# Kernel optimization log

Hardware: AMD Instinct MI355X
Metric: run time of the kernel (lower is better)

The kernel has to match this reference:

```python
import jax, jax.numpy as jnp
import numpy as np

EPS = 1e-5

def _layernorm(x, g, b):
    mu = jnp.mean(x, axis=-1, keepdims=True)
    var = jnp.mean((x - mu) ** 2, axis=-1, keepdims=True)
    return (x - mu) * jax.lax.rsqrt(var + EPS) * g + b


def setup_inputs() -> dict:
    key = jax.random.key(0)
    ks = jax.random.split(key, 16)
    B, N, D = 16, 10000, 64
    H = 4
    s = 0.02
    return {
        "z_m": jax.random.normal(ks[0], (B, N, D), jnp.float32),
        "z_c": jax.random.normal(ks[1], (B, N, D), jnp.float32),
        "z_t": jax.random.normal(ks[2], (B, N, D), jnp.float32),
        "z_cls": jax.random.normal(ks[3], (D,), jnp.float32) * s,
        # MultiheadAttention packed qkv projection: (3D, D) like torch in_proj_weight
        "in_proj_w": jax.random.normal(ks[4], (3 * D, D), jnp.float32) * s,
        "in_proj_b": jnp.zeros((3 * D,), jnp.float32),
        "out_w": jax.random.normal(ks[5], (D, D), jnp.float32) * s,  # torch (out,in)
        "out_b": jnp.zeros((D,), jnp.float32),
        "ln1_g": jnp.ones((D,), jnp.float32),
        "ln1_b": jnp.zeros((D,), jnp.float32),
        "ln2_g": jnp.ones((D,), jnp.float32),
        "ln2_b": jnp.zeros((D,), jnp.float32),
        "w1": jax.random.normal(ks[6], (2 * D, D), jnp.float32) * s,  # Linear(d, 2d), torch layout (out,in)
        "b1": jnp.zeros((2 * D,), jnp.float32),
        "w2": jax.random.normal(ks[7], (D, 2 * D), jnp.float32) * s,  # Linear(2d, d)
        "b2": jnp.zeros((D,), jnp.float32),
    }


def reference(z_m, z_c, z_t, z_cls, in_proj_w, in_proj_b, out_w, out_b,
              ln1_g, ln1_b, ln2_g, ln2_b, w1, b1, w2, b2):
    B, N, D = z_m.shape
    H = 4
    DH = D // H
    # build (B*N, 4, D) token sequences: [cls, mRNA, CNV, Meth]
    cls_tok = jnp.broadcast_to(z_cls, (B, N, 1, D))
    mods = jnp.stack([z_m, z_c, z_t], axis=2)            # (B,N,3,D)
    X = jnp.concatenate([cls_tok, mods], axis=2).reshape(B * N, 4, D)  # (M,4,D)

    xn = _layernorm(X, ln1_g, ln1_b)
    qkv = jnp.einsum('msd,ed->mse', xn, in_proj_w) + in_proj_b  # (M,4,3D)
    q, k, v = jnp.split(qkv, 3, axis=-1)
    # split heads -> (M,H,4,DH)
    def heads(t):
        return t.reshape(-1, 4, H, DH).transpose(0, 2, 1, 3)
    q, k, v = heads(q), heads(k), heads(v)
    scores = jnp.einsum('mhqd,mhkd->mhqk', q, k) / jnp.sqrt(jnp.float32(DH))
    attn = jax.nn.softmax(scores, axis=-1)               # (M,H,4,4)
    ctx = jnp.einsum('mhqk,mhkd->mhqd', attn, v)
    ctx = ctx.transpose(0, 2, 1, 3).reshape(-1, 4, D)
    attn_out = jnp.einsum('msd,ed->mse', ctx, out_w) + out_b
    # torch need_weights=True averages over heads by default -> (M,4,4)
    attn_weights = jnp.mean(attn, axis=1)

    X = X + attn_out
    yn = _layernorm(X, ln2_g, ln2_b)
    h1 = jax.nn.gelu(jnp.einsum('msd,ed->mse', yn, w1) + b1, approximate=False)
    X = X + jnp.einsum('mse,de->msd', h1, w2) + b2

    h_i = X.reshape(B, N, 4, D)[:, :, 0, :]
    return h_i, attn_weights
```

## Files before the change

### kernel.cpp

```cpp
#include <hip/hip_runtime.h>
#include <math.h>


typedef __attribute__((ext_vector_type(8))) short   short8;
typedef __attribute__((ext_vector_type(4))) float   f32x4;
typedef __attribute__((ext_vector_type(4))) unsigned short us4;
typedef __attribute__((ext_vector_type(8))) unsigned short us8;

#define MFMA16(a,b,c) __builtin_amdgcn_mfma_f32_16x16x32_bf16((a),(b),(c),0,0,0)
#define SWZ(b_, r_) (((unsigned)(b_)) ^ ((((unsigned)(r_)) & 7u) << 4))

__device__ __forceinline__ unsigned short f2bf(float f){
  union { float f; unsigned u; } v; v.f = f;
  unsigned r = v.u + 0x7FFFu + ((v.u >> 16) & 1u);
  return (unsigned short)(r >> 16);
}

__device__ __forceinline__ float fast_gelu(float a){
  float y = a * 0.70710678118654752f;
  float z = fabsf(y);
  float t = __frcp_rn(fmaf(0.3275911f, z, 1.f));
  float poly = t * fmaf(t, fmaf(t, fmaf(t, fmaf(t, 1.061405429f, -1.453152027f),
                                        1.421413741f), -0.284496736f), 0.254829592f);
  float e = __expf(-y * y);
  float erfz = 1.f - poly * e;
  float erfy = (y < 0.f) ? -erfz : erfz;
  return 0.5f * a * (1.f + erfy);
}

template<int C>
__device__ __forceinline__ void stage_w(const float* __restrict__ g,
                                        unsigned short* s, int R, int tid){
  for (int i = tid; i < R*C; i += 256){
    int row = i / C;
    s[SWZ((unsigned)i * 2u, row) >> 1] = f2bf(g[i]);
  }
}

__global__ __launch_bounds__(256)
__attribute__((amdgpu_waves_per_eu(2)))
void mt_kernel(const float* __restrict__ z_m, const float* __restrict__ z_c,
               const float* __restrict__ z_t, const float* __restrict__ z_cls,
               const float* __restrict__ ipw, const float* __restrict__ ipb,
               const float* __restrict__ out_w, const float* __restrict__ out_b,
               const float* __restrict__ ln1_g, const float* __restrict__ ln1_b,
               const float* __restrict__ ln2_g, const float* __restrict__ ln2_b,
               const float* __restrict__ w1, const float* __restrict__ b1,
               const float* __restrict__ w2, const float* __restrict__ b2,
               float* __restrict__ h_out, float* __restrict__ aw_out, int M)
{
  __shared__ unsigned short ipw_s[192*64];
  __shared__ unsigned short ow_s [64*64];
  __shared__ unsigned short w1_s [128*64];
  __shared__ unsigned short w2_s [64*128];
  __shared__ unsigned short xn_s [4*16*64];
  __shared__ unsigned short ctx_s[16*64];
  __shared__ unsigned short yn_s [16*64];
  __shared__ unsigned short h1_s [16*128];

  const int tid = threadIdx.x;
  const int w   = tid >> 6;
  const int l   = tid & 63;
  const int p   = l >> 4;
  const int c16 = l & 15;

  stage_w<64 >(ipw,   ipw_s, 192, tid);
  stage_w<64 >(out_w, ow_s,   64, tid);
  stage_w<64 >(w1,    w1_s,  128, tid);
  stage_w<128>(w2,    w2_s,   64, tid);
  __syncthreads();

  const int d0A = (l & 3) * 16;
  float ln1g[16], ln1b[16];
  #pragma unroll
  for (int i = 0; i < 16; ++i){ ln1g[i] = ln1_g[d0A+i]; ln1b[i] = ln1_b[d0A+i]; }
  float ipb_r[12];
  #pragma unroll
  for (int n = 0; n < 12; ++n) ipb_r[n] = ipb[c16 + 16*n];
  float zcob[16], ln2g[16], ln2b[16];
  #pragma unroll
  for (int mt = 0; mt < 4; ++mt)
    #pragma unroll
    for (int r = 0; r < 4; ++r){
      int e = 16*mt + 4*p + r;
      zcob[mt*4+r] = z_cls[e] + out_b[e];
      ln2g[mt*4+r] = ln2_g[e];  ln2b[mt*4+r] = ln2_b[e];
    }
  float b1r[8];
  #pragma unroll
  for (int tt = 0; tt < 2; ++tt)
    #pragma unroll
    for (int r = 0; r < 4; ++r) b1r[tt*4+r] = b1[16*(2*w+tt) + 4*p + r];
  float b2r[4];
  #pragma unroll
  for (int r = 0; r < 4; ++r) b2r[r] = b2[16*w + 4*p + r];

  unsigned short* xw = xn_s + w*1024;

  const int nT = M >> 4;
  for (int T = blockIdx.x; T < nT; T += gridDim.x){

    {
      const int t  = l >> 2;
      const int sq_ = t & 3;
      const int g  = t >> 2;
      const int m  = T*16 + 4*w + g;
      const float* srcp;
      if      (sq_ == 0) srcp = z_cls + d0A;
      else if (sq_ == 1) srcp = z_m + (size_t)m*64 + d0A;
      else if (sq_ == 2) srcp = z_c + (size_t)m*64 + d0A;
      else               srcp = z_t + (size_t)m*64 + d0A;
      float xv[16];
      #pragma unroll
      for (int i = 0; i < 4; ++i){
        float4 q4 = ((const float4*)srcp)[i];
        xv[4*i+0]=q4.x; xv[4*i+1]=q4.y; xv[4*i+2]=q4.z; xv[4*i+3]=q4.w;
      }
      float sm = 0.f;
      #pragma unroll
      for (int i = 0; i < 16; ++i) sm += xv[i];
      sm += __shfl_xor(sm, 1); sm += __shfl_xor(sm, 2);
      float mu = sm * (1.f/64.f);
      float sq = 0.f;
      #pragma unroll
      for (int i = 0; i < 16; ++i){ float d = xv[i]-mu; sq = fmaf(d,d,sq); }
      sq += __shfl_xor(sq, 1); sq += __shfl_xor(sq, 2);
      float rstd = 1.f / sqrtf(sq * (1.f/64.f) + 1e-5f);
      us8 v0, v1;
      #pragma unroll
      for (int i = 0; i < 8; ++i)
        v0[i] = f2bf(fmaf((xv[i]-mu)*rstd, ln1g[i], ln1b[i]));
      #pragma unroll
      for (int i = 0; i < 8; ++i)
        v1[i] = f2bf(fmaf((xv[8+i]-mu)*rstd, ln1g[8+i], ln1b[8+i]));
      unsigned b0 = (unsigned)(t*64 + d0A) * 2u;
      *(us8*)&xw[SWZ(b0,      t) >> 1] = v0;
      *(us8*)&xw[SWZ(b0 + 16, t) >> 1] = v1;
    }
    __syncthreads();

    f32x4 acc[12];
    #pragma unroll
    for (int n = 0; n < 12; ++n) acc[n] = (f32x4){0.f,0.f,0.f,0.f};
    {
      short8 a0 = *(const short8*)&xw[SWZ((c16*64 +      8*p)*2, c16) >> 1];
      short8 a1 = *(const short8*)&xw[SWZ((c16*64 + 32 + 8*p)*2, c16) >> 1];
      #pragma unroll
      for (int n = 0; n < 12; ++n){
        int e = c16 + 16*n;
        short8 b0 = *(const short8*)&ipw_s[SWZ((e*64 +      8*p)*2, e) >> 1];
        short8 b1v= *(const short8*)&ipw_s[SWZ((e*64 + 32 + 8*p)*2, e) >> 1];
        acc[n] = MFMA16(a0, b0, acc[n]);
        acc[n] = MFMA16(a1, b1v, acc[n]);
      }
      #pragma unroll
      for (int n = 0; n < 12; ++n){
        float bi = ipb_r[n];
        #pragma unroll
        for (int r = 0; r < 4; ++r) acc[n][r] += bi;
      }
    }

    float awm[16];
    #pragma unroll
    for (int i = 0; i < 16; ++i) awm[i] = 0.f;
    float ctx4[4];
    #pragma unroll
    for (int h = 0; h < 4; ++h){
      float sc[16];
      #pragma unroll
      for (int q = 0; q < 4; ++q)
        #pragma unroll
        for (int u = 0; u < 4; ++u) sc[q*4+u] = acc[h][q] * acc[4+h][u];
      #pragma unroll
      for (int st = 0; st < 4; ++st){
        const int mask = 1 << st;
        #pragma unroll
        for (int i = 0; i < 16; ++i) sc[i] += __shfl_xor(sc[i], mask);
      }
      #pragma unroll
      for (int q = 0; q < 4; ++q){
        float s0 = sc[4*q+0]*0.25f, s1 = sc[4*q+1]*0.25f,
              s2 = sc[4*q+2]*0.25f, s3 = sc[4*q+3]*0.25f;
        float mx = fmaxf(fmaxf(s0,s1), fmaxf(s2,s3));
        s0 = __expf(s0-mx); s1 = __expf(s1-mx); s2 = __expf(s2-mx); s3 = __expf(s3-mx);
        float inv = 1.f/(s0+s1+s2+s3);
        s0*=inv; s1*=inv; s2*=inv; s3*=inv;
        sc[4*q+0]=s0; sc[4*q+1]=s1; sc[4*q+2]=s2; sc[4*q+3]=s3;
        awm[4*q+0]+=s0; awm[4*q+1]+=s1; awm[4*q+2]+=s2; awm[4*q+3]+=s3;
      }
      ctx4[h] = sc[0]*acc[8+h][0] + sc[1]*acc[8+h][1]
              + sc[2]*acc[8+h][2] + sc[3]*acc[8+h][3];
    }
    {
      const int m0 = T*16 + 4*w + p;
      if (c16 == 0){
        float4* ap = (float4*)(aw_out + (size_t)m0*16);
        ap[0] = make_float4(awm[0]*0.25f, awm[1]*0.25f, awm[2]*0.25f, awm[3]*0.25f);
        ap[1] = make_float4(awm[4]*0.25f, awm[5]*0.25f, awm[6]*0.25f, awm[7]*0.25f);
        ap[2] = make_float4(awm[8]*0.25f, awm[9]*0.25f, awm[10]*0.25f, awm[11]*0.25f);
        ap[3] = make_float4(awm[12]*0.25f, awm[13]*0.25f, awm[14]*0.25f, awm[15]*0.25f);
      }
      const int grow = 4*w + p;
      #pragma unroll
      for (int h = 0; h < 4; ++h)
        ctx_s[SWZ((grow*64 + c16 + 16*h)*2, grow) >> 1] = f2bf(ctx4[h]);
    }
    __syncthreads();

    f32x4 op[4];
    #pragma unroll
    for (int mt = 0; mt < 4; ++mt) op[mt] = (f32x4){0.f,0.f,0.f,0.f};
    {
      short8 cb0 = *(const short8*)&ctx_s[SWZ((c16*64 +      8*p)*2, c16) >> 1];
      short8 cb1 = *(const short8*)&ctx_s[SWZ((c16*64 + 32 + 8*p)*2, c16) >> 1];
      #pragma unroll
      for (int mt = 0; mt < 4; ++mt){
        int er = 16*mt + c16;
        short8 a0 = *(const short8*)&ow_s[SWZ((er*64 +      8*p)*2, er) >> 1];
        short8 a1 = *(const short8*)&ow_s[SWZ((er*64 + 32 + 8*p)*2, er) >> 1];
        op[mt] = MFMA16(a0, cb0, op[mt]);
        op[mt] = MFMA16(a1, cb1, op[mt]);
      }
    }
    float x0[16], x0w[4];
    #pragma unroll
    for (int mt = 0; mt < 4; ++mt)
      #pragma unroll
      for (int r = 0; r < 4; ++r) x0[mt*4+r] = op[mt][r] + zcob[mt*4+r];
    #pragma unroll
    for (int mt = 0; mt < 4; ++mt)
      if (mt == w){
        #pragma unroll
        for (int r = 0; r < 4; ++r) x0w[r] = x0[mt*4+r];
      }
    float sm2 = 0.f;
    #pragma unroll
    for (int i = 0; i < 16; ++i) sm2 += x0[i];
    sm2 += __shfl_xor(sm2, 16); sm2 += __shfl_xor(sm2, 32);
    float mu2 = sm2 * (1.f/64.f);
    float sq2 = 0.f;
    #pragma unroll
    for (int i = 0; i < 16; ++i){ float d = x0[i]-mu2; sq2 = fmaf(d,d,sq2); }
    sq2 += __shfl_xor(sq2, 16); sq2 += __shfl_xor(sq2, 32);
    float rstd2 = 1.f / sqrtf(sq2 * (1.f/64.f) + 1e-5f);
    if (w == 0){
      #pragma unroll
      for (int mt = 0; mt < 4; ++mt){
        us4 v;
        #pragma unroll
        for (int r = 0; r < 4; ++r)
          v[r] = f2bf(fmaf((x0[mt*4+r]-mu2)*rstd2, ln2g[mt*4+r], ln2b[mt*4+r]));
        *(us4*)&yn_s[SWZ((c16*64 + 16*mt + 4*p)*2, c16) >> 1] = v;
      }
    }
    __syncthreads();

    f32x4 f1[2];
    #pragma unroll
    for (int tt = 0; tt < 2; ++tt) f1[tt] = (f32x4){0.f,0.f,0.f,0.f};
    {
      short8 yb0 = *(const short8*)&yn_s[SWZ((c16*64 +      8*p)*2, c16) >> 1];
      short8 yb1 = *(const short8*)&yn_s[SWZ((c16*64 + 32 + 8*p)*2, c16) >> 1];
      #pragma unroll
      for (int tt = 0; tt < 2; ++tt){
        int er = 16*(2*w+tt) + c16;
        short8 a0 = *(const short8*)&w1_s[SWZ((er*64 +      8*p)*2, er) >> 1];
        short8 a1 = *(const short8*)&w1_s[SWZ((er*64 + 32 + 8*p)*2, er) >> 1];
        f1[tt] = MFMA16(a0, yb0, f1[tt]);
        f1[tt] = MFMA16(a1, yb1, f1[tt]);
      }
    }
    #pragma unroll
    for (int tt = 0; tt < 2; ++tt){
      us4 v;
      #pragma unroll
      for (int r = 0; r < 4; ++r)
        v[r] = f2bf(fast_gelu(f1[tt][r] + b1r[tt*4+r]));
      *(us4*)&h1_s[SWZ((c16*128 + 16*(2*w+tt) + 4*p)*2, c16) >> 1] = v;
    }
    __syncthreads();

    f32x4 f2 = (f32x4){0.f,0.f,0.f,0.f};
    {
      int ar = 16*w + c16;
      #pragma unroll
      for (int ks = 0; ks < 4; ++ks){
        short8 a = *(const short8*)&w2_s[SWZ((ar*128 + 32*ks + 8*p)*2, ar) >> 1];
        short8 b = *(const short8*)&h1_s[SWZ((c16*128 + 32*ks + 8*p)*2, c16) >> 1];
        f2 = MFMA16(a, b, f2);
      }
    }
    float4 ov;
    ov.x = x0w[0] + b2r[0] + f2[0];
    ov.y = x0w[1] + b2r[1] + f2[1];
    ov.z = x0w[2] + b2r[2] + f2[2];
    ov.w = x0w[3] + b2r[3] + f2[3];
    *(float4*)(h_out + (size_t)(T*16 + c16)*64 + 16*w + 4*p) = ov;
  }
}

extern "C" void kernel_launch(void* const* d_in, const int* in_sizes, int n_in,
                              void* d_out, int out_size, void* d_ws, size_t ws_size,
                              hipStream_t stream) {
  const float* z_m   = (const float*)d_in[0];
  const float* z_c   = (const float*)d_in[1];
  const float* z_t   = (const float*)d_in[2];
  const float* z_cls = (const float*)d_in[3];
  const float* ipw   = (const float*)d_in[4];
  const float* ipb   = (const float*)d_in[5];
  const float* out_w = (const float*)d_in[6];
  const float* out_b = (const float*)d_in[7];
  const float* ln1_g = (const float*)d_in[8];
  const float* ln1_b = (const float*)d_in[9];
  const float* ln2_g = (const float*)d_in[10];
  const float* ln2_b = (const float*)d_in[11];
  const float* w1    = (const float*)d_in[12];
  const float* b1    = (const float*)d_in[13];
  const float* w2    = (const float*)d_in[14];
  const float* b2    = (const float*)d_in[15];

  const int M = in_sizes[0] / 64;
  float* h_out  = (float*)d_out;
  float* aw_out = h_out + (size_t)M * 64;

  const int nT = M >> 4;
  int grid = nT < 512 ? nT : 512;

  hipLaunchKernelGGL(mt_kernel, dim3(grid), dim3(256), 0, stream,
                     z_m, z_c, z_t, z_cls, ipw, ipb, out_w, out_b,
                     ln1_g, ln1_b, ln2_g, ln2_b, w1, b1, w2, b2,
                     h_out, aw_out, M);
}
```

Baseline: 397.9 us.

## Make each wave process independent 4-sample tiles without block barriers

Restructures the kernel so each wave owns four samples end to end, using a private LDS buffer instead of block-shared staging. This removes all per-tile __syncthreads. The LayerNorm gamma and beta are folded into the projection weights and biases at staging time. Blocks grow to 512 threads with fixed grid 512, and LN1 output feeds MFMA directly from registers. The cost is more redundant MFMA work per wave, since only 4 of 16 columns are useful. It also relies on implicit wave-level ordering for LDS reuse without barriers.

```diff
diff --git a/kernel.cpp b/kernel.cpp
--- a/kernel.cpp
+++ b/kernel.cpp
@@ -5,7 +5,6 @@
 typedef __attribute__((ext_vector_type(8))) short   short8;
 typedef __attribute__((ext_vector_type(4))) float   f32x4;
 typedef __attribute__((ext_vector_type(4))) unsigned short us4;
-typedef __attribute__((ext_vector_type(8))) unsigned short us8;
 
 #define MFMA16(a,b,c) __builtin_amdgcn_mfma_f32_16x16x32_bf16((a),(b),(c),0,0,0)
 #define SWZ(b_, r_) (((unsigned)(b_)) ^ ((((unsigned)(r_)) & 7u) << 4))
@@ -28,17 +27,8 @@
   return 0.5f * a * (1.f + erfy);
 }
 
-template<int C>
-__device__ __forceinline__ void stage_w(const float* __restrict__ g,
-                                        unsigned short* s, int R, int tid){
-  for (int i = tid; i < R*C; i += 256){
-    int row = i / C;
-    s[SWZ((unsigned)i * 2u, row) >> 1] = f2bf(g[i]);
-  }
-}
-
-__global__ __launch_bounds__(256)
-__attribute__((amdgpu_waves_per_eu(2)))
+__global__ __launch_bounds__(512)
+__attribute__((amdgpu_waves_per_eu(4, 4)))
 void mt_kernel(const float* __restrict__ z_m, const float* __restrict__ z_c,
                const float* __restrict__ z_t, const float* __restrict__ z_cls,
                const float* __restrict__ ipw, const float* __restrict__ ipb,
@@ -53,112 +43,114 @@
   __shared__ unsigned short ow_s [64*64];
   __shared__ unsigned short w1_s [128*64];
   __shared__ unsigned short w2_s [64*128];
-  __shared__ unsigned short xn_s [4*16*64];
-  __shared__ unsigned short ctx_s[16*64];
-  __shared__ unsigned short yn_s [16*64];
-  __shared__ unsigned short h1_s [16*128];
+  __shared__ float          par_s[448];
+  __shared__ unsigned short wbuf_s[8][512];
 
   const int tid = threadIdx.x;
-  const int w   = tid >> 6;
+
+  for (int i = tid; i < 192*64; i += 512){
+    int row = i >> 6;
+    ipw_s[SWZ((unsigned)i*2u, row) >> 1] = f2bf(ipw[i] * ln1_g[i & 63]);
+  }
+  for (int i = tid; i < 64*64; i += 512){
+    int row = i >> 6;
+    ow_s[SWZ((unsigned)i*2u, row) >> 1] = f2bf(out_w[i]);
+  }
+  for (int i = tid; i < 128*64; i += 512){
+    int row = i >> 6;
+    w1_s[SWZ((unsigned)i*2u, row) >> 1] = f2bf(w1[i] * ln2_g[i & 63]);
+  }
+  for (int i = tid; i < 64*128; i += 512){
+    int row = i >> 7;
+    w2_s[SWZ((unsigned)i*2u, row) >> 1] = f2bf(w2[i]);
+  }
+  for (int i = tid; i < 448; i += 512){
+    float v;
+    if (i < 192){
+      float a = ipb[i];
+      const float* wr = ipw + (size_t)i * 64;
+      #pragma unroll 4
+      for (int d = 0; d < 64; ++d) a = fmaf(wr[d], ln1_b[d], a);
+      v = a;
+    } else if (i < 256){
+      v = z_cls[i-192] + out_b[i-192];
+    } else if (i < 384){
+      int e = i - 256;
+      float a = b1[e];
+      const float* wr = w1 + (size_t)e * 64;
+      #pragma unroll 4
+      for (int d = 0; d < 64; ++d) a = fmaf(wr[d], ln2_b[d], a);
+      v = a;
+    } else {
+      v = b2[i-384];
+    }
+    par_s[i] = v;
+  }
+  __syncthreads();
+
+  const int w8  = tid >> 6;
   const int l   = tid & 63;
   const int p   = l >> 4;
   const int c16 = l & 15;
-
-  stage_w<64 >(ipw,   ipw_s, 192, tid);
-  stage_w<64 >(out_w, ow_s,   64, tid);
-  stage_w<64 >(w1,    w1_s,  128, tid);
-  stage_w<128>(w2,    w2_s,   64, tid);
-  __syncthreads();
-
-  const int d0A = (l & 3) * 16;
-  float ln1g[16], ln1b[16];
-  #pragma unroll
-  for (int i = 0; i < 16; ++i){ ln1g[i] = ln1_g[d0A+i]; ln1b[i] = ln1_b[d0A+i]; }
-  float ipb_r[12];
-  #pragma unroll
-  for (int n = 0; n < 12; ++n) ipb_r[n] = ipb[c16 + 16*n];
-  float zcob[16], ln2g[16], ln2b[16];
-  #pragma unroll
-  for (int mt = 0; mt < 4; ++mt)
-    #pragma unroll
-    for (int r = 0; r < 4; ++r){
-      int e = 16*mt + 4*p + r;
-      zcob[mt*4+r] = z_cls[e] + out_b[e];
-      ln2g[mt*4+r] = ln2_g[e];  ln2b[mt*4+r] = ln2_b[e];
-    }
-  float b1r[8];
-  #pragma unroll
-  for (int tt = 0; tt < 2; ++tt)
-    #pragma unroll
-    for (int r = 0; r < 4; ++r) b1r[tt*4+r] = b1[16*(2*w+tt) + 4*p + r];
-  float b2r[4];
-  #pragma unroll
-  for (int r = 0; r < 4; ++r) b2r[r] = b2[16*w + 4*p + r];
-
-  unsigned short* xw = xn_s + w*1024;
-
-  const int nT = M >> 4;
-  for (int T = blockIdx.x; T < nT; T += gridDim.x){
-
+  const int g4  = c16 & 3;
+  unsigned short* mybuf = wbuf_s[w8];
+
+  const int nWT    = M >> 2;
+  const int stride = gridDim.x * 8;
+  for (int wt = blockIdx.x*8 + w8; wt < nWT; wt += stride){
+
+    const int s_ = c16 & 3;
+    const int m  = wt*4 + (c16 >> 2);
+    const float* rowp;
+    if      (s_ == 0) rowp = z_cls;
+    else if (s_ == 1) rowp = z_m + (size_t)m * 64;
+    else if (s_ == 2) rowp = z_c + (size_t)m * 64;
+    else              rowp = z_t + (size_t)m * 64;
+
+    float xv[16];
     {
-      const int t  = l >> 2;
-      const int sq_ = t & 3;
-      const int g  = t >> 2;
-      const int m  = T*16 + 4*w + g;
-      const float* srcp;
-      if      (sq_ == 0) srcp = z_cls + d0A;
-      else if (sq_ == 1) srcp = z_m + (size_t)m*64 + d0A;
-      else if (sq_ == 2) srcp = z_c + (size_t)m*64 + d0A;
-      else               srcp = z_t + (size_t)m*64 + d0A;
-      float xv[16];
-      #pragma unroll
-      for (int i = 0; i < 4; ++i){
-        float4 q4 = ((const float4*)srcp)[i];
-        xv[4*i+0]=q4.x; xv[4*i+1]=q4.y; xv[4*i+2]=q4.z; xv[4*i+3]=q4.w;
-      }
-      float sm = 0.f;
-      #pragma unroll
-      for (int i = 0; i < 16; ++i) sm += xv[i];
-      sm += __shfl_xor(sm, 1); sm += __shfl_xor(sm, 2);
-      float mu = sm * (1.f/64.f);
-      float sq = 0.f;
-      #pragma unroll
-      for (int i = 0; i < 16; ++i){ float d = xv[i]-mu; sq = fmaf(d,d,sq); }
-      sq += __shfl_xor(sq, 1); sq += __shfl_xor(sq, 2);
-      float rstd = 1.f / sqrtf(sq * (1.f/64.f) + 1e-5f);
-      us8 v0, v1;
-      #pragma unroll
-      for (int i = 0; i < 8; ++i)
-        v0[i] = f2bf(fmaf((xv[i]-mu)*rstd, ln1g[i], ln1b[i]));
-      #pragma unroll
-      for (int i = 0; i < 8; ++i)
-        v1[i] = f2bf(fmaf((xv[8+i]-mu)*rstd, ln1g[8+i], ln1b[8+i]));
-      unsigned b0 = (unsigned)(t*64 + d0A) * 2u;
-      *(us8*)&xw[SWZ(b0,      t) >> 1] = v0;
-      *(us8*)&xw[SWZ(b0 + 16, t) >> 1] = v1;
-    }
-    __syncthreads();
+      float4 q0 = *(const float4*)(rowp + 8*p);
+      float4 q1 = *(const float4*)(rowp + 8*p + 4);
+      float4 q2 = *(const float4*)(rowp + 32 + 8*p);
+      float4 q3 = *(const float4*)(rowp + 32 + 8*p + 4);
+      xv[0]=q0.x; xv[1]=q0.y; xv[2]=q0.z; xv[3]=q0.w;
+      xv[4]=q1.x; xv[5]=q1.y; xv[6]=q1.z; xv[7]=q1.w;
+      xv[8]=q2.x; xv[9]=q2.y; xv[10]=q2.z; xv[11]=q2.w;
+      xv[12]=q3.x; xv[13]=q3.y; xv[14]=q3.z; xv[15]=q3.w;
+    }
+    float sm = 0.f;
+    #pragma unroll
+    for (int i = 0; i < 16; ++i) sm += xv[i];
+    sm += __shfl_xor(sm, 16); sm += __shfl_xor(sm, 32);
+    float mu = sm * (1.f/64.f);
+    float sq = 0.f;
+    #pragma unroll
+    for (int i = 0; i < 16; ++i){ float d = xv[i]-mu; sq = fmaf(d, d, sq); }
+    sq += __shfl_xor(sq, 16); sq += __shfl_xor(sq, 32);
+    float rstd = 1.f / sqrtf(sq * (1.f/64.f) + 1e-5f);
+
+    short8 a0, a1;
+    #pragma unroll
+    for (int j = 0; j < 8; ++j) a0[j] = (short)f2bf((xv[j]   - mu) * rstd);
+    #pragma unroll
+    for (int j = 0; j < 8; ++j) a1[j] = (short)f2bf((xv[8+j] - mu) * rstd);
 
     f32x4 acc[12];
     #pragma unroll
     for (int n = 0; n < 12; ++n) acc[n] = (f32x4){0.f,0.f,0.f,0.f};
-    {
-      short8 a0 = *(const short8*)&xw[SWZ((c16*64 +      8*p)*2, c16) >> 1];
-      short8 a1 = *(const short8*)&xw[SWZ((c16*64 + 32 + 8*p)*2, c16) >> 1];
-      #pragma unroll
-      for (int n = 0; n < 12; ++n){
-        int e = c16 + 16*n;
-        short8 b0 = *(const short8*)&ipw_s[SWZ((e*64 +      8*p)*2, e) >> 1];
-        short8 b1v= *(const short8*)&ipw_s[SWZ((e*64 + 32 + 8*p)*2, e) >> 1];
-        acc[n] = MFMA16(a0, b0, acc[n]);
-        acc[n] = MFMA16(a1, b1v, acc[n]);
-      }
-      #pragma unroll
-      for (int n = 0; n < 12; ++n){
-        float bi = ipb_r[n];
-        #pragma unroll
-        for (int r = 0; r < 4; ++r) acc[n][r] += bi;
-      }
+    #pragma unroll
+    for (int n = 0; n < 12; ++n){
+      int e = c16 + 16*n;
+      short8 b0 = *(const short8*)&ipw_s[SWZ((e*64 +      8*p)*2, e) >> 1];
+      short8 b1v= *(const short8*)&ipw_s[SWZ((e*64 + 32 + 8*p)*2, e) >> 1];
+      acc[n] = MFMA16(a0, b0, acc[n]);
+      acc[n] = MFMA16(a1, b1v, acc[n]);
+    }
+    #pragma unroll
+    for (int n = 0; n < 12; ++n){
+      float bi = par_s[c16 + 16*n];
+      #pragma unroll
+      for (int r = 0; r < 4; ++r) acc[n][r] += bi;
     }
 
     float awm[16];
@@ -192,48 +184,40 @@
       ctx4[h] = sc[0]*acc[8+h][0] + sc[1]*acc[8+h][1]
               + sc[2]*acc[8+h][2] + sc[3]*acc[8+h][3];
     }
-    {
-      const int m0 = T*16 + 4*w + p;
-      if (c16 == 0){
-        float4* ap = (float4*)(aw_out + (size_t)m0*16);
-        ap[0] = make_float4(awm[0]*0.25f, awm[1]*0.25f, awm[2]*0.25f, awm[3]*0.25f);
-        ap[1] = make_float4(awm[4]*0.25f, awm[5]*0.25f, awm[6]*0.25f, awm[7]*0.25f);
-        ap[2] = make_float4(awm[8]*0.25f, awm[9]*0.25f, awm[10]*0.25f, awm[11]*0.25f);
-        ap[3] = make_float4(awm[12]*0.25f, awm[13]*0.25f, awm[14]*0.25f, awm[15]*0.25f);
-      }
-      const int grow = 4*w + p;
-      #pragma unroll
-      for (int h = 0; h < 4; ++h)
-        ctx_s[SWZ((grow*64 + c16 + 16*h)*2, grow) >> 1] = f2bf(ctx4[h]);
-    }
-    __syncthreads();
+    if (c16 == 0){
+      float4* ap = (float4*)(aw_out + (size_t)(wt*4 + p)*16);
+      ap[0] = make_float4(awm[0]*0.25f,  awm[1]*0.25f,  awm[2]*0.25f,  awm[3]*0.25f);
+      ap[1] = make_float4(awm[4]*0.25f,  awm[5]*0.25f,  awm[6]*0.25f,  awm[7]*0.25f);
+      ap[2] = make_float4(awm[8]*0.25f,  awm[9]*0.25f,  awm[10]*0.25f, awm[11]*0.25f);
+      ap[3] = make_float4(awm[12]*0.25f, awm[13]*0.25f, awm[14]*0.25f, awm[15]*0.25f);
+    }
+
+    #pragma unroll
+    for (int h = 0; h < 4; ++h)
+      mybuf[p*64 + 16*h + c16] = f2bf(ctx4[h]);
+    short8 cb0 = *(const short8*)&mybuf[g4*64 +      8*p];
+    short8 cb1 = *(const short8*)&mybuf[g4*64 + 32 + 8*p];
 
     f32x4 op[4];
     #pragma unroll
     for (int mt = 0; mt < 4; ++mt) op[mt] = (f32x4){0.f,0.f,0.f,0.f};
-    {
-      short8 cb0 = *(const short8*)&ctx_s[SWZ((c16*64 +      8*p)*2, c16) >> 1];
-      short8 cb1 = *(const short8*)&ctx_s[SWZ((c16*64 + 32 + 8*p)*2, c16) >> 1];
-      #pragma unroll
-      for (int mt = 0; mt < 4; ++mt){
-        int er = 16*mt + c16;
-        short8 a0 = *(const short8*)&ow_s[SWZ((er*64 +      8*p)*2, er) >> 1];
-        short8 a1 = *(const short8*)&ow_s[SWZ((er*64 + 32 + 8*p)*2, er) >> 1];
-        op[mt] = MFMA16(a0, cb0, op[mt]);
-        op[mt] = MFMA16(a1, cb1, op[mt]);
-      }
-    }
-    float x0[16], x0w[4];
-    #pragma unroll
-    for (int mt = 0; mt < 4; ++mt)
-      #pragma unroll
-      for (int r = 0; r < 4; ++r) x0[mt*4+r] = op[mt][r] + zcob[mt*4+r];
-    #pragma unroll
-    for (int mt = 0; mt < 4; ++mt)
-      if (mt == w){
-        #pragma unroll
-        for (int r = 0; r < 4; ++r) x0w[r] = x0[mt*4+r];
-      }
+    #pragma unroll
+    for (int mt = 0; mt < 4; ++mt){
+      int er = 16*mt + c16;
+      short8 A0 = *(const short8*)&ow_s[SWZ((er*64 +      8*p)*2, er) >> 1];
+      short8 A1 = *(const short8*)&ow_s[SWZ((er*64 + 32 + 8*p)*2, er) >> 1];
+      op[mt] = MFMA16(A0, cb0, op[mt]);
+      op[mt] = MFMA16(A1, cb1, op[mt]);
+    }
+    float x0[16];
+    #pragma unroll
+    for (int mt = 0; mt < 4; ++mt){
+      float4 z4 = *(const float4*)&par_s[192 + 16*mt + 4*p];
+      x0[4*mt+0] = op[mt][0] + z4.x;
+      x0[4*mt+1] = op[mt][1] + z4.y;
+      x0[4*mt+2] = op[mt][2] + z4.z;
+      x0[4*mt+3] = op[mt][3] + z4.w;
+    }
     float sm2 = 0.f;
     #pragma unroll
     for (int i = 0; i < 16; ++i) sm2 += x0[i];
@@ -241,62 +225,72 @@
     float mu2 = sm2 * (1.f/64.f);
     float sq2 = 0.f;
     #pragma unroll
-    for (int i = 0; i < 16; ++i){ float d = x0[i]-mu2; sq2 = fmaf(d,d,sq2); }
+    for (int i = 0; i < 16; ++i){ float d = x0[i]-mu2; sq2 = fmaf(d, d, sq2); }
     sq2 += __shfl_xor(sq2, 16); sq2 += __shfl_xor(sq2, 32);
     float rstd2 = 1.f / sqrtf(sq2 * (1.f/64.f) + 1e-5f);
-    if (w == 0){
+    if (c16 < 4){
       #pragma unroll
       for (int mt = 0; mt < 4; ++mt){
         us4 v;
         #pragma unroll
         for (int r = 0; r < 4; ++r)
-          v[r] = f2bf(fmaf((x0[mt*4+r]-mu2)*rstd2, ln2g[mt*4+r], ln2b[mt*4+r]));
-        *(us4*)&yn_s[SWZ((c16*64 + 16*mt + 4*p)*2, c16) >> 1] = v;
-      }
-    }
-    __syncthreads();
-
-    f32x4 f1[2];
-    #pragma unroll
-    for (int tt = 0; tt < 2; ++tt) f1[tt] = (f32x4){0.f,0.f,0.f,0.f};
-    {
-      short8 yb0 = *(const short8*)&yn_s[SWZ((c16*64 +      8*p)*2, c16) >> 1];
-      short8 yb1 = *(const short8*)&yn_s[SWZ((c16*64 + 32 + 8*p)*2, c16) >> 1];
-      #pragma unroll
-      for (int tt = 0; tt < 2; ++tt){
-        int er = 16*(2*w+tt) + c16;
-        short8 a0 = *(const short8*)&w1_s[SWZ((er*64 +      8*p)*2, er) >> 1];
-        short8 a1 = *(const short8*)&w1_s[SWZ((er*64 + 32 + 8*p)*2, er) >> 1];
-        f1[tt] = MFMA16(a0, yb0, f1[tt]);
-        f1[tt] = MFMA16(a1, yb1, f1[tt]);
-      }
-    }
-    #pragma unroll
-    for (int tt = 0; tt < 2; ++tt){
-      us4 v;
-      #pragma unroll
-      for (int r = 0; r < 4; ++r)
-        v[r] = f2bf(fast_gelu(f1[tt][r] + b1r[tt*4+r]));
-      *(us4*)&h1_s[SWZ((c16*128 + 16*(2*w+tt) + 4*p)*2, c16) >> 1] = v;
-    }
-    __syncthreads();
-
-    f32x4 f2 = (f32x4){0.f,0.f,0.f,0.f};
-    {
-      int ar = 16*w + c16;
+          v[r] = f2bf((x0[4*mt+r] - mu2) * rstd2);
+        *(us4*)&mybuf[c16*64 + 16*mt + 4*p] = v;
+      }
+    }
+
+    short8 yb0 = *(const short8*)&mybuf[g4*64 +      8*p];
+    short8 yb1 = *(const short8*)&mybuf[g4*64 + 32 + 8*p];
+    f32x4 f1[8];
+    #pragma unroll
+    for (int mt = 0; mt < 8; ++mt) f1[mt] = (f32x4){0.f,0.f,0.f,0.f};
+    #pragma unroll
+    for (int mt = 0; mt < 8; ++mt){
+      int er = 16*mt + c16;
+      short8 A0 = *(const short8*)&w1_s[SWZ((er*64 +      8*p)*2, er) >> 1];
+      short8 A1 = *(const short8*)&w1_s[SWZ((er*64 + 32 + 8*p)*2, er) >> 1];
+      f1[mt] = MFMA16(A0, yb0, f1[mt]);
+      f1[mt] = MFMA16(A1, yb1, f1[mt]);
+    }
+    if (c16 < 4){
+      #pragma unroll
+      for (int mt = 0; mt < 8; ++mt){
+        float4 b4 = *(const float4*)&par_s[256 + 16*mt + 4*p];
+        us4 v;
+        v[0] = f2bf(fast_gelu(f1[mt][0] + b4.x));
+        v[1] = f2bf(fast_gelu(f1[mt][1] + b4.y));
+        v[2] = f2bf(fast_gelu(f1[mt][2] + b4.z));
+        v[3] = f2bf(fast_gelu(f1[mt][3] + b4.w));
+        *(us4*)&mybuf[c16*128 + 16*mt + 4*p] = v;
+      }
+    }
+
+    f32x4 f2a[4];
+    #pragma unroll
+    for (int mt = 0; mt < 4; ++mt) f2a[mt] = (f32x4){0.f,0.f,0.f,0.f};
+    #pragma unroll
+    for (int mt = 0; mt < 4; ++mt){
+      int ar = 16*mt + c16;
       #pragma unroll
       for (int ks = 0; ks < 4; ++ks){
-        short8 a = *(const short8*)&w2_s[SWZ((ar*128 + 32*ks + 8*p)*2, ar) >> 1];
-        short8 b = *(const short8*)&h1_s[SWZ((c16*128 + 32*ks + 8*p)*2, c16) >> 1];
-        f2 = MFMA16(a, b, f2);
-      }
-    }
-    float4 ov;
-    ov.x = x0w[0] + b2r[0] + f2[0];
-    ov.y = x0w[1] + b2r[1] + f2[1];
-    ov.z = x0w[2] + b2r[2] + f2[2];
-    ov.w = x0w[3] + b2r[3] + f2[3];
-    *(float4*)(h_out + (size_t)(T*16 + c16)*64 + 16*w + 4*p) = ov;
+        short8 A = *(const short8*)&w2_s[SWZ((ar*128 + 32*ks + 8*p)*2, ar) >> 1];
+        short8 B = *(const short8*)&mybuf[g4*128 + 32*ks + 8*p];
+        f2a[mt] = MFMA16(A, B, f2a[mt]);
+      }
+    }
+    if (c16 < 4){
+      float* orow = h_out + (size_t)(wt*4 + c16)*64;
+      #pragma unroll
+      for (int mt = 0; mt < 4; ++mt){
+        float4 b4 = *(const float4*)&par_s[384 + 16*mt + 4*p];
+        float4 ov;
+        ov.x = f2a[mt][0] + x0[4*mt+0] + b4.x;
+        ov.y = f2a[mt][1] + x0[4*mt+1] + b4.y;
+        ov.z = f2a[mt][2] + x0[4*mt+2] + b4.z;
+        ov.w = f2a[mt][3] + x0[4*mt+3] + b4.w;
+        *(float4*)(orow + 16*mt + 4*p) = ov;
+      }
+    }
   }
 }
 
@@ -324,10 +318,7 @@
   float* h_out  = (float*)d_out;
   float* aw_out = h_out + (size_t)M * 64;
 
-  const int nT = M >> 4;
-  int grid = nT < 512 ? nT : 512;
-
-  hipLaunchKernelGGL(mt_kernel, dim3(grid), dim3(256), 0, stream,
+  hipLaunchKernelGGL(mt_kernel, dim3(512), dim3(512), 0, stream,
                      z_m, z_c, z_t, z_cls, ipw, ipb, out_w, out_b,
                      ln1_g, ln1_b, ln2_g, ln2_b, w1, b1, w2, b2,
                      h_out, aw_out, M);
```

New measurement: 441.8 us. 11.0% more time.
